# Kernel tuning notes

Hardware: AMD Instinct MI355X
Metric: run time of the kernel (lower is better)

## Reference

```python
import jax, jax.numpy as jnp
import numpy as np

NUM_NEURONS = 65536
T_STEPS = 1024
V_TH = 1.0
V_RESET = 0.0
TAU = 20.0
DT = 1.0


def setup_inputs() -> dict:
    key = jax.random.key(0)
    input_current = jax.random.normal(key, (T_STEPS, NUM_NEURONS), dtype=jnp.float32)
    return {"input_current": input_current}


def reference(input_current) -> jnp.ndarray:
    """LIF recurrence. The original loops over the batch axis while each
    neuron object carries membrane potential V across rows, so the batch
    axis is sequential (time). Vectorized over neurons, lax.scan over time.

    V <- V + dt/tau * (-(V - V_reset) + I)
    spike = V >= V_th ; V <- V_reset where spiked
    """
    alpha = jnp.float32(DT / TAU)

    def step(V, I):
        V = V + alpha * (V_RESET - V + I)
        spike = V >= V_TH
        V = jnp.where(spike, jnp.float32(V_RESET), V)
        return V, spike.astype(jnp.float32)

    V0 = jnp.full((input_current.shape[1],), V_RESET, dtype=jnp.float32)
    _, spikes = jax.lax.scan(step, V0, input_current)
    return spikes  # (T, N) binary float32
```

## Files before the change

### kernel.cpp

```cpp
#include <hip/hip_runtime.h>


#define T_STEPS 1024
#define NUM_NEURONS 65536
#define VEC 4
#define NVEC (NUM_NEURONS / VEC)
#define BLOCK 64
#define UNROLL 16

typedef float f4 __attribute__((ext_vector_type(4)));

__global__ __launch_bounds__(BLOCK) void lif_kernel(const f4* __restrict__ in,
                                                    f4* __restrict__ out) {
    const int gid = blockIdx.x * BLOCK + threadIdx.x;
    constexpr float alpha = 0.05f;
    constexpr float vth = 1.0f;

    float vx = 0.0f, vy = 0.0f, vz = 0.0f, vw = 0.0f;
    const f4* __restrict__ p = in + gid;
    f4* __restrict__ q = out + gid;

    for (int t = 0; t < T_STEPS; t += UNROLL) {
        f4 I[UNROLL];
#pragma unroll
        for (int u = 0; u < UNROLL; ++u) {
            I[u] = p[(size_t)(t + u) * NVEC];
        }
#pragma unroll
        for (int u = 0; u < UNROLL; ++u) {
            f4 c = I[u];
            vx = vx + alpha * (c.x - vx);
            vy = vy + alpha * (c.y - vy);
            vz = vz + alpha * (c.z - vz);
            vw = vw + alpha * (c.w - vw);
            f4 s;
            s.x = (vx >= vth) ? 1.0f : 0.0f;
            s.y = (vy >= vth) ? 1.0f : 0.0f;
            s.z = (vz >= vth) ? 1.0f : 0.0f;
            s.w = (vw >= vth) ? 1.0f : 0.0f;
            vx = (vx >= vth) ? 0.0f : vx;
            vy = (vy >= vth) ? 0.0f : vy;
            vz = (vz >= vth) ? 0.0f : vz;
            vw = (vw >= vth) ? 0.0f : vw;
            __builtin_nontemporal_store(s, q + (size_t)(t + u) * NVEC);
        }
    }
}

extern "C" void kernel_launch(void* const* d_in, const int* in_sizes, int n_in,
                              void* d_out, int out_size, void* d_ws, size_t ws_size,
                              hipStream_t stream) {
    const f4* in = (const f4*)d_in[0];
    f4* out = (f4*)d_out;
    lif_kernel<<<NVEC / BLOCK, BLOCK, 0, stream>>>(in, out);
}
```

Baseline: 474.9 us.

## Use scalar per-thread neurons with register double-buffered input prefetch

Switches from four neurons per thread (float4) to one neuron per thread with 256-thread blocks, which gives four times as many threads and waves. Loads for the next chunk of 16 time steps are issued into a second register buffer before the current chunk is computed, so memory latency overlaps with the compute and store chain. The cost is narrower 4-byte accesses in place of 16-byte vector loads and stores, which means more memory instructions.

```diff
diff --git a/kernel.cpp b/kernel.cpp
--- a/kernel.cpp
+++ b/kernel.cpp
@@ -2,55 +2,53 @@
 
 
 #define T_STEPS 1024
+#define N NUM_NEURONS
 #define NUM_NEURONS 65536
-#define VEC 4
-#define NVEC (NUM_NEURONS / VEC)
-#define BLOCK 64
-#define UNROLL 16
+#define BLOCK 256
+#define U 16
 
-typedef float f4 __attribute__((ext_vector_type(4)));
-
-__global__ __launch_bounds__(BLOCK) void lif_kernel(const f4* __restrict__ in,
-                                                    f4* __restrict__ out) {
+__global__ __launch_bounds__(BLOCK) void lif_kernel(const float* __restrict__ in,
+                                                    float* __restrict__ out) {
     const int gid = blockIdx.x * BLOCK + threadIdx.x;
     constexpr float alpha = 0.05f;
     constexpr float vth = 1.0f;
 
-    float vx = 0.0f, vy = 0.0f, vz = 0.0f, vw = 0.0f;
-    const f4* __restrict__ p = in + gid;
-    f4* __restrict__ q = out + gid;
+    float V = 0.0f;
+    const float* __restrict__ p = in + gid;
+    float* __restrict__ q = out + gid;
 
-    for (int t = 0; t < T_STEPS; t += UNROLL) {
-        f4 I[UNROLL];
+    float I[U], J[U];
+
 #pragma unroll
-        for (int u = 0; u < UNROLL; ++u) {
-            I[u] = p[(size_t)(t + u) * NVEC];
+    for (int u = 0; u < U; ++u) I[u] = p[(size_t)u * N];
+
+    for (int t = 0; t < T_STEPS - U; t += U) {
+#pragma unroll
+        for (int u = 0; u < U; ++u) J[u] = p[(size_t)(t + U + u) * N];
+#pragma unroll
+        for (int u = 0; u < U; ++u) {
+            V = V + alpha * (I[u] - V);
+            float s = (V >= vth) ? 1.0f : 0.0f;
+            V = (V >= vth) ? 0.0f : V;
+            __builtin_nontemporal_store(s, q + (size_t)(t + u) * N);
         }
 #pragma unroll
-        for (int u = 0; u < UNROLL; ++u) {
-            f4 c = I[u];
-            vx = vx + alpha * (c.x - vx);
-            vy = vy + alpha * (c.y - vy);
-            vz = vz + alpha * (c.z - vz);
-            vw = vw + alpha * (c.w - vw);
-            f4 s;
-            s.x = (vx >= vth) ? 1.0f : 0.0f;
-            s.y = (vy >= vth) ? 1.0f : 0.0f;
-            s.z = (vz >= vth) ? 1.0f : 0.0f;
-            s.w = (vw >= vth) ? 1.0f : 0.0f;
-            vx = (vx >= vth) ? 0.0f : vx;
-            vy = (vy >= vth) ? 0.0f : vy;
-            vz = (vz >= vth) ? 0.0f : vz;
-            vw = (vw >= vth) ? 0.0f : vw;
-            __builtin_nontemporal_store(s, q + (size_t)(t + u) * NVEC);
-        }
+        for (int u = 0; u < U; ++u) I[u] = J[u];
+    }
+
+#pragma unroll
+    for (int u = 0; u < U; ++u) {
+        V = V + alpha * (I[u] - V);
+        float s = (V >= vth) ? 1.0f : 0.0f;
+        V = (V >= vth) ? 0.0f : V;
+        __builtin_nontemporal_store(s, q + (size_t)(T_STEPS - U + u) * N);
     }
 }
 
 extern "C" void kernel_launch(void* const* d_in, const int* in_sizes, int n_in,
                               void* d_out, int out_size, void* d_ws, size_t ws_size,
                               hipStream_t stream) {
-    const f4* in = (const f4*)d_in[0];
-    f4* out = (f4*)d_out;
-    lif_kernel<<<NVEC / BLOCK, BLOCK, 0, stream>>>(in, out);
+    const float* in = (const float*)d_in[0];
+    float* out = (float*)d_out;
+    lif_kernel<<<NUM_NEURONS / BLOCK, BLOCK, 0, stream>>>(in, out);
 }
```

After: 427.0 us. -10.1%, faster.
